# Optimization experiments

Measured on AMD Instinct MI355X. Metric: run time of the kernel, lower is better.

Reference implementation:

```python
import jax, jax.numpy as jnp
import numpy as np

N_A, N_B = 100000, 100000
N = N_A + N_B
E = 600000
D_IN_A, D_IN_B = 64, 96
HID, OUT = 128, 64
R, BASES = 4, 4


def setup_inputs() -> dict:
    key = jax.random.key(0)
    ks = jax.random.split(key, 16)
    inp = {
        "x_author": jax.random.normal(ks[0], (N_A, D_IN_A), jnp.float32),
        "x_paper": jax.random.normal(ks[1], (N_B, D_IN_B), jnp.float32),
        "src": jax.random.randint(ks[2], (E,), 0, N, jnp.int32),
        "dst": jax.random.randint(ks[3], (E,), 0, N, jnp.int32),
        "edge_type": jax.random.randint(ks[4], (E,), 0, R, jnp.int32),
        # per-node-type linear projections (with bias, as nn.Linear)
        "W_proj_a": jax.random.normal(ks[5], (D_IN_A, HID), jnp.float32) / np.sqrt(D_IN_A),
        "b_proj_a": jnp.zeros((HID,), jnp.float32),
        "W_proj_b": jax.random.normal(ks[6], (D_IN_B, HID), jnp.float32) / np.sqrt(D_IN_B),
        "b_proj_b": jnp.zeros((HID,), jnp.float32),
        # conv0: hid->hid, root_weight=False
        "basis0": jax.random.normal(ks[7], (BASES, HID, HID), jnp.float32) / np.sqrt(HID),
        "comp0": jax.random.normal(ks[8], (R, BASES), jnp.float32) / np.sqrt(BASES),
        # conv1: hid->hid, root_weight=True
        "basis1": jax.random.normal(ks[9], (BASES, HID, HID), jnp.float32) / np.sqrt(HID),
        "comp1": jax.random.normal(ks[10], (R, BASES), jnp.float32) / np.sqrt(BASES),
        "root1": jax.random.normal(ks[11], (HID, HID), jnp.float32) / np.sqrt(HID),
        # conv2: hid->out, root_weight=True
        "basis2": jax.random.normal(ks[12], (BASES, HID, OUT), jnp.float32) / np.sqrt(HID),
        "comp2": jax.random.normal(ks[13], (R, BASES), jnp.float32) / np.sqrt(BASES),
        "root2": jax.random.normal(ks[14], (HID, OUT), jnp.float32) / np.sqrt(HID),
    }
    return inp


def rgcn_conv(x, src, dst, etype, basis, comp, root):
    # basis-decomposed relation weights: [R, in, out]
    W = jnp.einsum('rb,bio->rio', comp, basis)
    out = jnp.zeros((x.shape[0], W.shape[2]), x.dtype)
    for r in range(R):  # small fixed relation count
        xw = x @ W[r]                                  # [N, out]
        m = (etype == r)
        msg = jnp.where(m[:, None], xw[src], 0.0)      # [E, out]
        s = jax.ops.segment_sum(msg, dst, num_segments=x.shape[0])
        cnt = jax.ops.segment_sum(m.astype(x.dtype), dst, num_segments=x.shape[0])
        out = out + s / jnp.maximum(cnt, 1.0)[:, None]  # per-relation mean aggr
    if root is not None:
        out = out + x @ root
    return out


def reference(x_author, x_paper, src, dst, edge_type,
              W_proj_a, b_proj_a, W_proj_b, b_proj_b,
              basis0, comp0, basis1, comp1, root1, basis2, comp2, root2):
    # per-node-type projection + relu, then concat in node_type order
    ha = jax.nn.relu(x_author @ W_proj_a + b_proj_a)
    hp = jax.nn.relu(x_paper @ W_proj_b + b_proj_b)
    x = jnp.concatenate([ha, hp], axis=0)             # [N, HID]
    x_lat0 = x
    # dropout skipped (eval mode)
    x = jax.nn.relu(rgcn_conv(x, src, dst, edge_type, basis0, comp0, None))
    x_lat1 = x
    x = jax.nn.relu(rgcn_conv(x, src, dst, edge_type, basis1, comp1, root1))
    x_lat2 = x
    x = rgcn_conv(x, src, dst, edge_type, basis2, comp2, root2)
    return (x, x_lat0, x_lat1, x_lat2)
```

## Files before the change

kernel.cpp:

```cpp
#include <hip/hip_runtime.h>

constexpr int NNODES = 200000;
constexpr int NAUT   = 100000;
constexpr int NEDGE  = 600000;
constexpr int HIDC   = 128;
constexpr int OUTCH  = 64;
constexpr int RELS   = 4;
constexpr int SCAN_N = RELS * NNODES;
constexpr int LDB    = HIDC + 8;

typedef __attribute__((ext_vector_type(8))) short bf16x8;
typedef __attribute__((ext_vector_type(4))) float f32x4;

__device__ __forceinline__ unsigned short f2bf(float f) {
    unsigned int b = __float_as_uint(f);
    b += 0x7FFFu + ((b >> 16) & 1u);
    return (unsigned short)(b >> 16);
}
__device__ __forceinline__ float bf2f(unsigned short u) {
    return __uint_as_float(((unsigned int)u) << 16);
}

__device__ __forceinline__ int fragoff(int k, int n, int NB) {
    return ((k >> 5) * NB + (n >> 4)) * 512 + (((k >> 3) & 3) * 16 + (n & 15)) * 8 + (k & 7);
}


__global__ void count_kernel(const int* __restrict__ dst, const int* __restrict__ et,
                             int* __restrict__ bins) {
    int e = blockIdx.x * 256 + threadIdx.x;
    if (e < NEDGE) atomicAdd(&bins[et[e] * NNODES + dst[e]], 1);
}

__global__ void scan1_kernel(int* __restrict__ bins, int* __restrict__ blockSums) {
    __shared__ int s[256];
    int b = blockIdx.x, t = threadIdx.x;
    int base = b * 1024 + t * 4;
    int v[4], sum = 0;
#pragma unroll
    for (int i = 0; i < 4; i++) {
        v[i] = (base + i < SCAN_N) ? bins[base + i] : 0;
        sum += v[i];
    }
    s[t] = sum;
    __syncthreads();
    for (int off = 1; off < 256; off <<= 1) {
        int x = (t >= off) ? s[t - off] : 0;
        __syncthreads();
        if (t >= off) s[t] += x;
        __syncthreads();
    }
    int run = s[t] - sum;
    if (t == 255) blockSums[b] = s[255];
#pragma unroll
    for (int i = 0; i < 4; i++) {
        if (base + i < SCAN_N) bins[base + i] = run;
        run += v[i];
    }
}

__global__ void scan2_kernel(int* __restrict__ blockSums, int nb) {
    __shared__ int s[256];
    int t = threadIdx.x;
    int carry = 0;
    for (int base = 0; base < nb; base += 256) {
        int v = (base + t < nb) ? blockSums[base + t] : 0;
        s[t] = v;
        __syncthreads();
        for (int off = 1; off < 256; off <<= 1) {
            int x = (t >= off) ? s[t - off] : 0;
            __syncthreads();
            if (t >= off) s[t] += x;
            __syncthreads();
        }
        if (base + t < nb) blockSums[base + t] = carry + (s[t] - v);
        int total = s[255];
        __syncthreads();
        carry += total;
    }
}

__global__ void scan3_kernel(int* __restrict__ bins, const int* __restrict__ blockSums,
                             int* __restrict__ binCur) {
    int i = blockIdx.x * 256 + threadIdx.x;
    if (i < SCAN_N) {
        int v = bins[i] + blockSums[i >> 10];
        bins[i] = v;
        binCur[i] = v;
    }
}

__global__ void scatter_kernel(const int* __restrict__ src, const int* __restrict__ dst,
                               const int* __restrict__ et, int* __restrict__ binCur,
                               int* __restrict__ srcSorted) {
    int e = blockIdx.x * 256 + threadIdx.x;
    if (e < NEDGE) {
        int bin = et[e] * NNODES + dst[e];
        int pos = atomicAdd(&binCur[bin], 1);
        srcSorted[pos] = src[e];
    }
}

__global__ void fragify_kernel(const float* __restrict__ basis0, const float* __restrict__ comp0,
                               const float* __restrict__ basis1, const float* __restrict__ comp1,
                               const float* __restrict__ root1,
                               const float* __restrict__ basis2, const float* __restrict__ comp2,
                               const float* __restrict__ root2,
                               short* __restrict__ whi0, short* __restrict__ wlo0,
                               short* __restrict__ whi1, short* __restrict__ wlo1,
                               short* __restrict__ whiR1, short* __restrict__ wloR1,
                               short* __restrict__ whi2, short* __restrict__ wlo2,
                               short* __restrict__ whiR2, short* __restrict__ wloR2) {
    int idx = blockIdx.x * 256 + threadIdx.x;
    if (idx >= 188416) return;
    float w;
    short *hp, *lp;
    if (idx < 65536) {
        int r = idx >> 14, e = idx & 16383;
        int k = e >> 7, n = e & 127;
        w = 0.f;
#pragma unroll
        for (int b = 0; b < 4; b++) w += comp0[r * 4 + b] * basis0[b * 16384 + e];
        int off = r * 16384 + fragoff(k, n, 8);
        hp = whi0 + off; lp = wlo0 + off;
    } else if (idx < 131072) {
        int i2 = idx - 65536;
        int r = i2 >> 14, e = i2 & 16383;
        int k = e >> 7, n = e & 127;
        w = 0.f;
#pragma unroll
        for (int b = 0; b < 4; b++) w += comp1[r * 4 + b] * basis1[b * 16384 + e];
        int off = r * 16384 + fragoff(k, n, 8);
        hp = whi1 + off; lp = wlo1 + off;
    } else if (idx < 147456) {
        int e = idx - 131072;
        int k = e >> 7, n = e & 127;
        w = root1[e];
        int off = fragoff(k, n, 8);
        hp = whiR1 + off; lp = wloR1 + off;
    } else if (idx < 180224) {
        int i2 = idx - 147456;
        int r = i2 >> 13, e = i2 & 8191;
        int k = e >> 6, n = e & 63;
        w = 0.f;
#pragma unroll
        for (int b = 0; b < 4; b++) w += comp2[r * 4 + b] * basis2[b * 8192 + e];
        int off = r * 8192 + fragoff(k, n, 4);
        hp = whi2 + off; lp = wlo2 + off;
    } else {
        int e = idx - 180224;
        int k = e >> 6, n = e & 63;
        w = root2[e];
        int off = fragoff(k, n, 4);
        hp = whiR2 + off; lp = wloR2 + off;
    }
    unsigned short h = f2bf(w);
    unsigned short l = f2bf(w - bf2f(h));
    *hp = (short)h;
    *lp = (short)l;
}

__global__ __launch_bounds__(256) void gemm_kernel(const float* __restrict__ A,
                                                   const float* __restrict__ B,
                                                   const float* __restrict__ bias,
                                                   float* __restrict__ C, int M, int K) {
    __shared__ float sA[64 * 128];
    int tid = threadIdx.x;
    int row0 = blockIdx.x * 64;

    for (int i = tid; i < (64 * K) >> 2; i += 256) {
        int off = i << 2;
        int rr = off / K, cc = off % K;
        int row = row0 + rr;
        float4 v = {0.f, 0.f, 0.f, 0.f};
        if (row < M) v = *(const float4*)(A + (long)row * K + cc);
        *(float4*)(sA + rr * K + cc) = v;
    }
    __syncthreads();

    int cg = tid & 31, rg = tid >> 5;
    int c0 = cg * 4, r0 = rg * 8;
    float acc[8][4];
#pragma unroll
    for (int i = 0; i < 8; i++)
#pragma unroll
        for (int j = 0; j < 4; j++) acc[i][j] = 0.f;

#pragma unroll 2
    for (int k = 0; k < K; k += 4) {
        float a[8][4];
#pragma unroll
        for (int i = 0; i < 8; i++)
            *(float4*)(a[i]) = *(const float4*)(sA + (r0 + i) * K + k);
#pragma unroll
        for (int j = 0; j < 4; j++) {
            float b[4];
            *(float4*)b = *(const float4*)(B + (k + j) * 128 + c0);
#pragma unroll
            for (int i = 0; i < 8; i++)
#pragma unroll
                for (int jj = 0; jj < 4; jj++)
                    acc[i][jj] = fmaf(a[i][j], b[jj], acc[i][jj]);
        }
    }

#pragma unroll
    for (int i = 0; i < 8; i++) {
        int row = row0 + r0 + i;
        if (row >= M) continue;
        float v[4];
#pragma unroll
        for (int jj = 0; jj < 4; jj++) v[jj] = fmaxf(acc[i][jj] + bias[c0 + jj], 0.f);
        *(float4*)(C + (long)row * 128 + c0) = *(float4*)v;
    }
}

template <int NC, bool HASROOT, bool DORELU>
__global__ __launch_bounds__(256) void conv_kernel(const float* __restrict__ x,
                                                   const short* __restrict__ whiRel,
                                                   const short* __restrict__ wloRel,
                                                   const short* __restrict__ whiRoot,
                                                   const short* __restrict__ wloRoot,
                                                   const int* __restrict__ binStart,
                                                   const int* __restrict__ binEnd,
                                                   const int* __restrict__ srcSorted,
                                                   float* __restrict__ out) {
    constexpr int NB  = NC / 16;
    constexpr int KB  = HIDC / 32;
    constexpr int TPW = NB / 4;
    __shared__ short sHi[64 * LDB];
    __shared__ short sLo[64 * LDB];
    int tid = threadIdx.x;
    int v0 = blockIdx.x * 64;

    const int grow = tid >> 2, gq = tid & 3;
    const int wave = tid >> 6, lane = tid & 63;
    const int lrow = lane & 15, lgrp = lane >> 4;

    f32x4 acc[4][TPW];
#pragma unroll
    for (int rt = 0; rt < 4; rt++)
#pragma unroll
        for (int t = 0; t < TPW; t++) acc[rt][t] = (f32x4){0.f, 0.f, 0.f, 0.f};

    constexpr int NPHASE = HASROOT ? RELS + 1 : RELS;
#pragma unroll 1
    for (int ph = 0; ph < NPHASE; ph++) {
        if (ph > 0) __syncthreads();
        if (ph < RELS) {
            int bin = ph * NNODES + v0 + grow;
            int s = binStart[bin], e = binEnd[bin];
            float4 a4[8];
#pragma unroll
            for (int i = 0; i < 8; i++) a4[i] = make_float4(0.f, 0.f, 0.f, 0.f);
            for (int j = s; j < e; j++) {
                const float* xs = x + (long)srcSorted[j] * HIDC;
#pragma unroll
                for (int i = 0; i < 8; i++) {
                    float4 v = *(const float4*)(xs + (gq + i * 4) * 4);
                    a4[i].x += v.x; a4[i].y += v.y; a4[i].z += v.z; a4[i].w += v.w;
                }
            }
            float sc = 1.0f / (float)max(e - s, 1);
#pragma unroll
            for (int i = 0; i < 8; i++) {
                float4 w = a4[i];
                w.x *= sc; w.y *= sc; w.z *= sc; w.w *= sc;
                unsigned short h0 = f2bf(w.x), h1 = f2bf(w.y), h2 = f2bf(w.z), h3 = f2bf(w.w);
                unsigned short l0 = f2bf(w.x - bf2f(h0)), l1 = f2bf(w.y - bf2f(h1));
                unsigned short l2 = f2bf(w.z - bf2f(h2)), l3 = f2bf(w.w - bf2f(h3));
                int c = (gq + i * 4) * 4;
                uint2 hv = make_uint2((unsigned)h0 | ((unsigned)h1 << 16),
                                      (unsigned)h2 | ((unsigned)h3 << 16));
                uint2 lv = make_uint2((unsigned)l0 | ((unsigned)l1 << 16),
                                      (unsigned)l2 | ((unsigned)l3 << 16));
                *(uint2*)(sHi + grow * LDB + c) = hv;
                *(uint2*)(sLo + grow * LDB + c) = lv;
            }
        } else {
#pragma unroll
            for (int i = 0; i < 8; i++) {
                int i4 = tid + 256 * i;
                int row = i4 >> 5, col4 = i4 & 31;
                float4 w = *(const float4*)(x + (long)(v0 + row) * HIDC + col4 * 4);
                unsigned short h0 = f2bf(w.x), h1 = f2bf(w.y), h2 = f2bf(w.z), h3 = f2bf(w.w);
                unsigned short l0 = f2bf(w.x - bf2f(h0)), l1 = f2bf(w.y - bf2f(h1));
                unsigned short l2 = f2bf(w.z - bf2f(h2)), l3 = f2bf(w.w - bf2f(h3));
                int c = col4 * 4;
                uint2 hv = make_uint2((unsigned)h0 | ((unsigned)h1 << 16),
                                      (unsigned)h2 | ((unsigned)h3 << 16));
                uint2 lv = make_uint2((unsigned)l0 | ((unsigned)l1 << 16),
                                      (unsigned)l2 | ((unsigned)l3 << 16));
                *(uint2*)(sHi + row * LDB + c) = hv;
                *(uint2*)(sLo + row * LDB + c) = lv;
            }
        }
        __syncthreads();

        const short* __restrict__ bhB = (ph < RELS) ? (whiRel + ph * (KB * NB * 512)) : whiRoot;
        const short* __restrict__ blB = (ph < RELS) ? (wloRel + ph * (KB * NB * 512)) : wloRoot;

#pragma unroll
        for (int kb = 0; kb < KB; kb++) {
            bf16x8 bh[TPW], bl[TPW];
#pragma unroll
            for (int t = 0; t < TPW; t++) {
                int nb = wave * TPW + t;
                int boff = ((kb * NB + nb) * 64 + lane) * 8;
                bh[t] = *(const bf16x8*)(bhB + boff);
                bl[t] = *(const bf16x8*)(blB + boff);
            }
#pragma unroll
            for (int rt = 0; rt < 4; rt++) {
                int aoff = (rt * 16 + lrow) * LDB + kb * 32 + lgrp * 8;
                bf16x8 ah = *(const bf16x8*)(sHi + aoff);
                bf16x8 al = *(const bf16x8*)(sLo + aoff);
#pragma unroll
                for (int t = 0; t < TPW; t++) {
                    acc[rt][t] = __builtin_amdgcn_mfma_f32_16x16x32_bf16(ah, bh[t], acc[rt][t], 0, 0, 0);
                    acc[rt][t] = __builtin_amdgcn_mfma_f32_16x16x32_bf16(al, bh[t], acc[rt][t], 0, 0, 0);
                    acc[rt][t] = __builtin_amdgcn_mfma_f32_16x16x32_bf16(ah, bl[t], acc[rt][t], 0, 0, 0);
                }
            }
        }
    }

#pragma unroll
    for (int rt = 0; rt < 4; rt++)
#pragma unroll
        for (int t = 0; t < TPW; t++) {
            int nb = wave * TPW + t;
            int col = nb * 16 + lrow;
#pragma unroll
            for (int j = 0; j < 4; j++) {
                float vv = acc[rt][t][j];
                if (DORELU) vv = fmaxf(vv, 0.f);
                out[(long)(v0 + rt * 16 + lgrp * 4 + j) * NC + col] = vv;
            }
        }
}


extern "C" void kernel_launch(void* const* d_in, const int* in_sizes, int n_in,
                              void* d_out, int out_size, void* d_ws, size_t ws_size,
                              hipStream_t stream) {
    const float* xa     = (const float*)d_in[0];
    const float* xp     = (const float*)d_in[1];
    const int*   src    = (const int*)d_in[2];
    const int*   dst    = (const int*)d_in[3];
    const int*   et     = (const int*)d_in[4];
    const float* Wpa    = (const float*)d_in[5];
    const float* bpa    = (const float*)d_in[6];
    const float* Wpb    = (const float*)d_in[7];
    const float* bpb    = (const float*)d_in[8];
    const float* basis0 = (const float*)d_in[9];
    const float* comp0  = (const float*)d_in[10];
    const float* basis1 = (const float*)d_in[11];
    const float* comp1  = (const float*)d_in[12];
    const float* root1  = (const float*)d_in[13];
    const float* basis2 = (const float*)d_in[14];
    const float* comp2  = (const float*)d_in[15];
    const float* root2  = (const float*)d_in[16];

    float* out_final = (float*)d_out;
    float* x0 = out_final + (size_t)NNODES * OUTCH;
    float* x1 = x0 + (size_t)NNODES * HIDC;
    float* x2 = x1 + (size_t)NNODES * HIDC;

    int* bins      = (int*)d_ws;
    int* binCur    = bins + SCAN_N;
    int* blockSums = binCur + SCAN_N;
    int* srcSorted = blockSums + 800;
    short* whi0  = (short*)(srcSorted + NEDGE);
    short* wlo0  = whi0 + 65536;
    short* whi1  = wlo0 + 65536;
    short* wlo1  = whi1 + 65536;
    short* whiR1 = wlo1 + 65536;
    short* wloR1 = whiR1 + 16384;
    short* whi2  = wloR1 + 16384;
    short* wlo2  = whi2 + 32768;
    short* whiR2 = wlo2 + 32768;
    short* wloR2 = whiR2 + 8192;

    dim3 b256(256);
    int egrid = (NEDGE + 255) / 256;
    int nScanBlocks = (SCAN_N + 1023) / 1024;

    hipMemsetAsync(bins, 0, (size_t)SCAN_N * sizeof(int), stream);
    hipLaunchKernelGGL(count_kernel, dim3(egrid), b256, 0, stream, dst, et, bins);
    hipLaunchKernelGGL(scan1_kernel, dim3(nScanBlocks), b256, 0, stream, bins, blockSums);
    hipLaunchKernelGGL(scan2_kernel, dim3(1), b256, 0, stream, blockSums, nScanBlocks);
    hipLaunchKernelGGL(scan3_kernel, dim3((SCAN_N + 255) / 256), b256, 0, stream,
                       bins, blockSums, binCur);
    hipLaunchKernelGGL(scatter_kernel, dim3(egrid), b256, 0, stream,
                       src, dst, et, binCur, srcSorted);

    hipLaunchKernelGGL(fragify_kernel, dim3((188416 + 255) / 256), b256, 0, stream,
                       basis0, comp0, basis1, comp1, root1, basis2, comp2, root2,
                       whi0, wlo0, whi1, wlo1, whiR1, wloR1, whi2, wlo2, whiR2, wloR2);

    hipLaunchKernelGGL(gemm_kernel, dim3((NAUT + 63) / 64), b256, 0, stream,
                       xa, Wpa, bpa, x0, NAUT, 64);
    hipLaunchKernelGGL(gemm_kernel, dim3((NAUT + 63) / 64), b256, 0, stream,
                       xp, Wpb, bpb, x0 + (size_t)NAUT * HIDC, NAUT, 96);

    int cgrid = NNODES / 64;

    hipLaunchKernelGGL((conv_kernel<128, false, true>), dim3(cgrid), b256, 0, stream,
                       x0, whi0, wlo0, (const short*)nullptr, (const short*)nullptr,
                       bins, binCur, srcSorted, x1);
    hipLaunchKernelGGL((conv_kernel<128, true, true>), dim3(cgrid), b256, 0, stream,
                       x1, whi1, wlo1, whiR1, wloR1, bins, binCur, srcSorted, x2);
    hipLaunchKernelGGL((conv_kernel<64, true, false>), dim3(cgrid), b256, 0, stream,
                       x2, whi2, wlo2, whiR2, wloR2, bins, binCur, srcSorted, out_final);
}
```

Before: 979.5 us.

## Double conv block threads to 512 and split MFMA tiles across eight waves

The conv kernel now launches 512 threads per 64-node block. Each node's gather is split across 8 threads instead of 4, and each wave owns one 16-row tile and half the columns, rather than all rows for a column slice. The gather loop also prefetches the next source index before loading the current row. The aim is more latency hiding in the irregular gather and higher occupancy, with launch_bounds(512,8). The cost is that B fragments are reloaded by more waves, and register pressure under the tighter bound may limit the gain.

```diff
diff --git a/kernel.cpp b/kernel.cpp
--- a/kernel.cpp
+++ b/kernel.cpp
@@ -216,32 +216,31 @@
 }
 
 template <int NC, bool HASROOT, bool DORELU>
-__global__ __launch_bounds__(256) void conv_kernel(const float* __restrict__ x,
-                                                   const short* __restrict__ whiRel,
-                                                   const short* __restrict__ wloRel,
-                                                   const short* __restrict__ whiRoot,
-                                                   const short* __restrict__ wloRoot,
-                                                   const int* __restrict__ binStart,
-                                                   const int* __restrict__ binEnd,
-                                                   const int* __restrict__ srcSorted,
-                                                   float* __restrict__ out) {
+__global__ __launch_bounds__(512, 8) void conv_kernel(const float* __restrict__ x,
+                                                      const short* __restrict__ whiRel,
+                                                      const short* __restrict__ wloRel,
+                                                      const short* __restrict__ whiRoot,
+                                                      const short* __restrict__ wloRoot,
+                                                      const int* __restrict__ binStart,
+                                                      const int* __restrict__ binEnd,
+                                                      const int* __restrict__ srcSorted,
+                                                      float* __restrict__ out) {
     constexpr int NB  = NC / 16;
     constexpr int KB  = HIDC / 32;
-    constexpr int TPW = NB / 4;
+    constexpr int TPW = NB / 2;
     __shared__ short sHi[64 * LDB];
     __shared__ short sLo[64 * LDB];
     int tid = threadIdx.x;
     int v0 = blockIdx.x * 64;
 
-    const int grow = tid >> 2, gq = tid & 3;
+    const int grow = tid >> 3, gq = tid & 7;
     const int wave = tid >> 6, lane = tid & 63;
     const int lrow = lane & 15, lgrp = lane >> 4;
-
-    f32x4 acc[4][TPW];
-#pragma unroll
-    for (int rt = 0; rt < 4; rt++)
-#pragma unroll
-        for (int t = 0; t < TPW; t++) acc[rt][t] = (f32x4){0.f, 0.f, 0.f, 0.f};
+    const int rt = wave >> 1, ch = wave & 1;
+
+    f32x4 acc[TPW];
+#pragma unroll
+    for (int t = 0; t < TPW; t++) acc[t] = (f32x4){0.f, 0.f, 0.f, 0.f};
 
     constexpr int NPHASE = HASROOT ? RELS + 1 : RELS;
 #pragma unroll 1
@@ -250,26 +249,31 @@
         if (ph < RELS) {
             int bin = ph * NNODES + v0 + grow;
             int s = binStart[bin], e = binEnd[bin];
-            float4 a4[8];
-#pragma unroll
-            for (int i = 0; i < 8; i++) a4[i] = make_float4(0.f, 0.f, 0.f, 0.f);
-            for (int j = s; j < e; j++) {
-                const float* xs = x + (long)srcSorted[j] * HIDC;
-#pragma unroll
-                for (int i = 0; i < 8; i++) {
-                    float4 v = *(const float4*)(xs + (gq + i * 4) * 4);
+            float4 a4[4];
+#pragma unroll
+            for (int i = 0; i < 4; i++) a4[i] = make_float4(0.f, 0.f, 0.f, 0.f);
+            int j = s;
+            int idx = (j < e) ? srcSorted[j] : 0;
+            while (j < e) {
+                int nidx = (j + 1 < e) ? srcSorted[j + 1] : 0;
+                const float* xs = x + (long)idx * HIDC;
+#pragma unroll
+                for (int i = 0; i < 4; i++) {
+                    float4 v = *(const float4*)(xs + (gq + i * 8) * 4);
                     a4[i].x += v.x; a4[i].y += v.y; a4[i].z += v.z; a4[i].w += v.w;
                 }
+                idx = nidx;
+                ++j;
             }
             float sc = 1.0f / (float)max(e - s, 1);
 #pragma unroll
-            for (int i = 0; i < 8; i++) {
+            for (int i = 0; i < 4; i++) {
                 float4 w = a4[i];
                 w.x *= sc; w.y *= sc; w.z *= sc; w.w *= sc;
                 unsigned short h0 = f2bf(w.x), h1 = f2bf(w.y), h2 = f2bf(w.z), h3 = f2bf(w.w);
                 unsigned short l0 = f2bf(w.x - bf2f(h0)), l1 = f2bf(w.y - bf2f(h1));
                 unsigned short l2 = f2bf(w.z - bf2f(h2)), l3 = f2bf(w.w - bf2f(h3));
-                int c = (gq + i * 4) * 4;
+                int c = (gq + i * 8) * 4;
                 uint2 hv = make_uint2((unsigned)h0 | ((unsigned)h1 << 16),
                                       (unsigned)h2 | ((unsigned)h3 << 16));
                 uint2 lv = make_uint2((unsigned)l0 | ((unsigned)l1 << 16),
@@ -279,8 +283,8 @@
             }
         } else {
 #pragma unroll
-            for (int i = 0; i < 8; i++) {
-                int i4 = tid + 256 * i;
+            for (int i = 0; i < 4; i++) {
+                int i4 = tid + 512 * i;
                 int row = i4 >> 5, col4 = i4 & 31;
                 float4 w = *(const float4*)(x + (long)(v0 + row) * HIDC + col4 * 4);
                 unsigned short h0 = f2bf(w.x), h1 = f2bf(w.y), h2 = f2bf(w.z), h3 = f2bf(w.w);
@@ -302,42 +306,33 @@
 
 #pragma unroll
         for (int kb = 0; kb < KB; kb++) {
-            bf16x8 bh[TPW], bl[TPW];
+            int aoff = (rt * 16 + lrow) * LDB + kb * 32 + lgrp * 8;
+            bf16x8 ah = *(const bf16x8*)(sHi + aoff);
+            bf16x8 al = *(const bf16x8*)(sLo + aoff);
 #pragma unroll
             for (int t = 0; t < TPW; t++) {
-                int nb = wave * TPW + t;
+                int nb = ch * TPW + t;
                 int boff = ((kb * NB + nb) * 64 + lane) * 8;
-                bh[t] = *(const bf16x8*)(bhB + boff);
-                bl[t] = *(const bf16x8*)(blB + boff);
-            }
-#pragma unroll
-            for (int rt = 0; rt < 4; rt++) {
-                int aoff = (rt * 16 + lrow) * LDB + kb * 32 + lgrp * 8;
-                bf16x8 ah = *(const bf16x8*)(sHi + aoff);
-                bf16x8 al = *(const bf16x8*)(sLo + aoff);
-#pragma unroll
-                for (int t = 0; t < TPW; t++) {
-                    acc[rt][t] = __builtin_amdgcn_mfma_f32_16x16x32_bf16(ah, bh[t], acc[rt][t], 0, 0, 0);
-                    acc[rt][t] = __builtin_amdgcn_mfma_f32_16x16x32_bf16(al, bh[t], acc[rt][t], 0, 0, 0);
-                    acc[rt][t] = __builtin_amdgcn_mfma_f32_16x16x32_bf16(ah, bl[t], acc[rt][t], 0, 0, 0);
-                }
+                bf16x8 bh = *(const bf16x8*)(bhB + boff);
+                bf16x8 bl = *(const bf16x8*)(blB + boff);
+                acc[t] = __builtin_amdgcn_mfma_f32_16x16x32_bf16(ah, bh, acc[t], 0, 0, 0);
+                acc[t] = __builtin_amdgcn_mfma_f32_16x16x32_bf16(al, bh, acc[t], 0, 0, 0);
+                acc[t] = __builtin_amdgcn_mfma_f32_16x16x32_bf16(ah, bl, acc[t], 0, 0, 0);
             }
         }
     }
 
 #pragma unroll
-    for (int rt = 0; rt < 4; rt++)
-#pragma unroll
-        for (int t = 0; t < TPW; t++) {
-            int nb = wave * TPW + t;
-            int col = nb * 16 + lrow;
-#pragma unroll
-            for (int j = 0; j < 4; j++) {
-                float vv = acc[rt][t][j];
-                if (DORELU) vv = fmaxf(vv, 0.f);
-                out[(long)(v0 + rt * 16 + lgrp * 4 + j) * NC + col] = vv;
-            }
+    for (int t = 0; t < TPW; t++) {
+        int nb = ch * TPW + t;
+        int col = nb * 16 + lrow;
+#pragma unroll
+        for (int j = 0; j < 4; j++) {
+            float vv = acc[t][j];
+            if (DORELU) vv = fmaxf(vv, 0.f);
+            out[(long)(v0 + rt * 16 + lgrp * 4 + j) * NC + col] = vv;
         }
+    }
 }
 
 
@@ -383,6 +378,7 @@
     short* wloR2 = whiR2 + 8192;
 
     dim3 b256(256);
+    dim3 b512(512);
     int egrid = (NEDGE + 255) / 256;
     int nScanBlocks = (SCAN_N + 1023) / 1024;
 
@@ -406,11 +402,11 @@
 
     int cgrid = NNODES / 64;
 
-    hipLaunchKernelGGL((conv_kernel<128, false, true>), dim3(cgrid), b256, 0, stream,
+    hipLaunchKernelGGL((conv_kernel<128, false, true>), dim3(cgrid), b512, 0, stream,
                        x0, whi0, wlo0, (const short*)nullptr, (const short*)nullptr,
                        bins, binCur, srcSorted, x1);
-    hipLaunchKernelGGL((conv_kernel<128, true, true>), dim3(cgrid), b256, 0, stream,
+    hipLaunchKernelGGL((conv_kernel<128, true, true>), dim3(cgrid), b512, 0, stream,
                        x1, whi1, wlo1, whiR1, wloR1, bins, binCur, srcSorted, x2);
-    hipLaunchKernelGGL((conv_kernel<64, true, false>), dim3(cgrid), b256, 0, stream,
+    hipLaunchKernelGGL((conv_kernel<64, true, false>), dim3(cgrid), b512, 0, stream,
                        x2, whi2, wlo2, whiR2, wloR2, bins, binCur, srcSorted, out_final);
 }
```

New measurement: 1.243 ms. 26.9% more time.
